# Kernel tuning notes

Hardware: AMD Instinct MI355X
Metric: run time of the kernel (lower is better)

The kernel has to match this reference:

```python
import math
import jax, jax.numpy as jnp
import numpy as np

B, S, HID, NH = 1, 2048, 4096, 32
HD = HID // NH  # 128
INV_NORM = 1.0 / math.sqrt(HD)


def _build_alibi(n_heads, seq_len, batch):
    # Standard Bloom ALiBi slopes.
    cp2 = 2 ** math.floor(math.log2(n_heads))
    base = 2.0 ** (-(2.0 ** -(math.log2(cp2) - 3)))
    slopes = base ** np.arange(1, cp2 + 1)
    if cp2 != n_heads:
        extra_base = 2.0 ** (-(2.0 ** -(math.log2(2 * cp2) - 3)))
        n_rem = min(cp2, n_heads - cp2)
        slopes = np.concatenate([slopes, extra_base ** np.arange(1, 2 * n_rem + 1, 2)])
    arange = np.arange(seq_len, dtype=np.float32)[None, None, :]
    alibi = slopes[:, None, None].astype(np.float32) * arange  # [NH,1,S]
    alibi = np.broadcast_to(alibi[None], (batch, n_heads, 1, seq_len)).reshape(batch * n_heads, 1, seq_len)
    return jnp.asarray(alibi, jnp.float32)


def setup_inputs() -> dict:
    key = jax.random.key(0)
    ks = jax.random.split(key, 5)
    return {
        "hidden_states": jax.random.normal(ks[0], (B, S, HID), jnp.float32),
        "alibi": _build_alibi(NH, S, B),  # [B*NH, 1, S]
        "w_qkv": jax.random.normal(ks[1], (3 * HID, HID), jnp.float32) * 0.02,
        "b_qkv": jax.random.normal(ks[2], (3 * HID,), jnp.float32) * 0.02,
        "w_dense": jax.random.normal(ks[3], (HID, HID), jnp.float32) * 0.02,
        "b_dense": jax.random.normal(ks[4], (HID,), jnp.float32) * 0.02,
    }


def reference(hidden_states, alibi, w_qkv, b_qkv, w_dense, b_dense):
    b, s, _ = hidden_states.shape
    # Fused QKV projection, per-head interleaved layout [B,S,NH,3,HD]
    fused = hidden_states @ w_qkv.T + b_qkv
    fused = fused.reshape(b, s, NH, 3, HD)
    q = fused[..., 0, :].transpose(0, 2, 1, 3).reshape(b * NH, s, HD)
    k = fused[..., 1, :].transpose(0, 2, 1, 3).reshape(b * NH, s, HD)
    v = fused[..., 2, :].transpose(0, 2, 1, 3).reshape(b * NH, s, HD)
    # baddbmm(alibi, q, k^T, beta=1.0, alpha=inv_norm_factor)
    scores = alibi + INV_NORM * jnp.einsum("bqd,bkd->bqk", q, k)  # [B*NH,S,S]
    causal = jnp.tril(jnp.ones((s, s), dtype=bool))
    scores = jnp.where(causal[None], scores, jnp.finfo(scores.dtype).min)
    probs = jax.nn.softmax(scores.astype(jnp.float32), axis=-1).astype(hidden_states.dtype)
    ctx = jnp.einsum("bqk,bkd->bqd", probs, v)  # [B*NH,S,HD]
    ctx = ctx.reshape(b, NH, s, HD).transpose(0, 2, 1, 3).reshape(b, s, HID)
    return ctx @ w_dense.T + b_dense
```

## Files before the change

### kernel.cpp

```cpp
#include <hip/hip_runtime.h>
#include <math.h>


typedef __attribute__((ext_vector_type(8))) short short8;
typedef __attribute__((ext_vector_type(4))) float floatx4;
typedef __attribute__((ext_vector_type(4))) unsigned short ushort4v;

#define S_LEN 2048
#define HID_DIM 4096
#define NHEADS 32
#define HDIM 128
#define QKV_N 12288
#define QK_STRIDE 8192
#define INV_NORM 0.08838834764831845f

__device__ __forceinline__ unsigned short f2bf(float f) {
    union { float f; unsigned int i; } v; v.f = f;
    unsigned int u = v.i;
    return (unsigned short)((u + 0x7fffu + ((u >> 16) & 1u)) >> 16);
}

typedef __attribute__((address_space(1))) unsigned int guint;
typedef __attribute__((address_space(3))) unsigned int luint;
__device__ __forceinline__ void gl_lds16(const unsigned short* g, unsigned short* l) {
    __builtin_amdgcn_global_load_lds((guint*)g, (luint*)l, 16, 0, 0);
}

__device__ __forceinline__ void wvm8() { asm volatile("s_waitcnt vmcnt(8)" ::: "memory"); }
__device__ __forceinline__ void wvm6() { asm volatile("s_waitcnt vmcnt(6)" ::: "memory"); }
__device__ __forceinline__ void wvm4() { asm volatile("s_waitcnt vmcnt(4)" ::: "memory"); }
__device__ __forceinline__ void wvm3() { asm volatile("s_waitcnt vmcnt(3)" ::: "memory"); }
__device__ __forceinline__ void wvm0() { asm volatile("s_waitcnt vmcnt(0)" ::: "memory"); }

__device__ __forceinline__ void phase_bar() {
    __builtin_amdgcn_s_barrier();
    __builtin_amdgcn_sched_barrier(0);
}

__global__ __launch_bounds__(256) void cvt_bf16(
    const float* __restrict__ src, unsigned short* __restrict__ dst)
{
    size_t i = ((size_t)blockIdx.x * 256 + threadIdx.x) * 8;
    float4 x = *(const float4*)(src + i);
    float4 y = *(const float4*)(src + i + 4);
    union { unsigned u[4]; short8 s; } r;
    r.u[0] = (unsigned)f2bf(x.x) | ((unsigned)f2bf(x.y) << 16);
    r.u[1] = (unsigned)f2bf(x.z) | ((unsigned)f2bf(x.w) << 16);
    r.u[2] = (unsigned)f2bf(y.x) | ((unsigned)f2bf(y.y) << 16);
    r.u[3] = (unsigned)f2bf(y.z) | ((unsigned)f2bf(y.w) << 16);
    *(short8*)(dst + i) = r.s;
}

template <int MODE, int BM>
__global__ __launch_bounds__(512, 2) void gemm_pipe(
    const unsigned short* __restrict__ A,
    const unsigned short* __restrict__ B,
    const float* __restrict__ bias,
    unsigned short* __restrict__ Cq,
    float* __restrict__ Cf,
    unsigned short* __restrict__ vt,
    int M, int N, int K)
{
    constexpr int BN = 256;
    constexpr int BK = 32;
    constexpr int MF = BM / 32;
    constexpr int WR = BM / 2;
    constexpr int BUFSH = (BM + BN) * BK;
    constexpr int LA = (BM * BK * 2) / 8192;

    __shared__ unsigned short lds[4 * BUFSH];

    const int t = threadIdx.x;
    const int w = t >> 6, lane = t & 63, quad = lane >> 4, l15 = lane & 15;
    const int wr = w >> 2, wc = w & 3;

    const int gx = gridDim.x;
    const int nwg = gx * gridDim.y;
    const int wg = blockIdx.y * gx + blockIdx.x;
    const int swz = (wg & 7) * (nwg >> 3) + (wg >> 3);
    const int bx = swz % gx, by = swz / gx;
    const int mb = by * BM, nb = bx * BN;

    const int srow = w * 16 + (lane >> 2);
    const int schunk = (((lane & 3) ^ ((lane >> 2) & 3)) << 3);
    const unsigned short* pa = A + (size_t)(mb + srow) * K + schunk;
    const unsigned short* pb = B + (size_t)(nb + srow) * K + schunk;
    const int la_off = w * 512;
    const int lb_off = BM * BK + w * 512;

    const int fchunk = ((quad ^ (l15 & 3)) << 3);
    const int aoff = (wr * WR + l15) * BK + fchunk;
    const int boff = BM * BK + (wc * 64 + l15) * BK + fchunk;

    floatx4 acc[MF][4];
#pragma unroll
    for (int i = 0; i < MF; i++)
#pragma unroll
        for (int j = 0; j < 4; j++) acc[i][j] = (floatx4)0.0f;

    int kstage = 0;
    auto stage = [&](int bufi) {
        unsigned short* lb = &lds[bufi * BUFSH];
#pragma unroll
        for (int i = 0; i < LA; i++)
            gl_lds16(pa + kstage + (size_t)i * 128 * K, lb + la_off + i * 4096);
        gl_lds16(pb + kstage, lb + lb_off);
        gl_lds16(pb + kstage + (size_t)128 * K, lb + lb_off + 4096);
        kstage += BK;
    };
    auto compute = [&](int bufi) {
        const unsigned short* lt = &lds[bufi * BUFSH];
        short8 af[MF], bfr[4];
#pragma unroll
        for (int m = 0; m < MF; m++)
            af[m] = *(const short8*)&lt[aoff + m * 16 * BK];
#pragma unroll
        for (int n = 0; n < 4; n++)
            bfr[n] = *(const short8*)&lt[boff + n * 16 * BK];
        __builtin_amdgcn_s_setprio(1);
#pragma unroll
        for (int m = 0; m < MF; m++)
#pragma unroll
            for (int n = 0; n < 4; n++)
                acc[m][n] = __builtin_amdgcn_mfma_f32_16x16x32_bf16(af[m], bfr[n], acc[m][n], 0, 0, 0);
        __builtin_amdgcn_s_setprio(0);
    };

    const int NT = K / BK;

    stage(0); stage(1); stage(2);

    for (int kt = 0; kt < NT - 2; kt++) {
        if constexpr (BM == 256) wvm8(); else wvm6();
        phase_bar();
        if (kt < NT - 3) stage((kt + 3) & 3);
        compute(kt & 3);
    }
    if constexpr (BM == 256) wvm4(); else wvm3();
    phase_bar();
    compute((NT - 2) & 3);
    wvm0();
    phase_bar();
    compute((NT - 1) & 3);

    if (MODE == 1) {
#pragma unroll
        for (int j = 0; j < 4; j++) {
            int cb = nb + wc * 64 + j * 16;
            int h = cb / 384;
            int type = (cb >> 7) % 3;
            int db = cb & 127;
            float bv = bias[cb + l15];
            if (type == 2) {
                unsigned short* vp = vt + ((size_t)h * HDIM + db + l15) * S_LEN;
#pragma unroll
                for (int m = 0; m < MF; m++) {
                    int rowbase = mb + wr * WR + m * 16 + quad * 4;
                    ushort4v pk;
#pragma unroll
                    for (int r = 0; r < 4; r++) pk[r] = f2bf(acc[m][j][r] + bv);
                    *(ushort4v*)&vp[rowbase] = pk;
                }
            } else {
                size_t colo = (size_t)h * 256 + type * 128 + db + l15;
#pragma unroll
                for (int m = 0; m < MF; m++) {
                    int rowbase = mb + wr * WR + m * 16 + quad * 4;
#pragma unroll
                    for (int r = 0; r < 4; r++)
                        Cq[(size_t)(rowbase + r) * QK_STRIDE + colo] =
                            f2bf(acc[m][j][r] + bv);
                }
            }
        }
    } else {
#pragma unroll
        for (int j = 0; j < 4; j++) {
            int col = nb + wc * 64 + j * 16 + l15;
            float bv = bias[col];
#pragma unroll
            for (int m = 0; m < MF; m++) {
                int rowbase = mb + wr * WR + m * 16 + quad * 4;
#pragma unroll
                for (int r = 0; r < 4; r++)
                    Cf[(size_t)(rowbase + r) * N + col] = acc[m][j][r] + bv;
            }
        }
    }
}

__global__ __launch_bounds__(256) void attn_flash(
    const unsigned short* __restrict__ qk,
    const unsigned short* __restrict__ vt,
    const float* __restrict__ alibi,
    unsigned short* __restrict__ ctx)
{
    __shared__ unsigned short k_lds[64 * 136];
    __shared__ unsigned short vt_lds[128 * 72];
    __shared__ unsigned short p_lds[4 * 16 * 72];

    int h = blockIdx.x;
    int qb = blockIdx.y * 64;
    int t = threadIdx.x;
    int w = t >> 6, lane = t & 63, quad = lane >> 4, l15 = lane & 15;
    int qoff = h * 256;

    short8 qf[4];
    {
        int qrow = qb + w * 16 + l15;
        const unsigned short* qp = qk + (size_t)qrow * QK_STRIDE + qoff;
        for (int ks = 0; ks < 4; ks++)
            qf[ks] = *(const short8*)&qp[ks * 32 + quad * 8];
    }

    floatx4 o[8];
    for (int j = 0; j < 8; j++) o[j] = (floatx4)0.0f;
    float m_prev[4], l_prev[4];
    for (int r = 0; r < 4; r++) { m_prev[r] = -INFINITY; l_prev[r] = 0.0f; }

    int ntiles = qb / 64 + 1;
    for (int tile = 0; tile < ntiles; tile++) {
        int kb = tile * 64;
        for (int i = 0; i < 4; i++) {
            int idx = t + 256 * i;
            int krow = idx >> 4, kcol = (idx & 15) * 8;
            *(short8*)&k_lds[krow * 136 + kcol] =
                *(const short8*)(qk + (size_t)(kb + krow) * QK_STRIDE + qoff + 128 + kcol);
            int d = idx >> 3, ch = (idx & 7) * 8;
            *(short8*)&vt_lds[d * 72 + ch] =
                *(const short8*)(vt + ((size_t)h * HDIM + d) * S_LEN + kb + ch);
        }
        __syncthreads();

        floatx4 s[4];
        for (int j = 0; j < 4; j++) s[j] = (floatx4)0.0f;
        for (int ks = 0; ks < 4; ks++) {
            for (int j = 0; j < 4; j++) {
                short8 bfr = *(const short8*)&k_lds[(j * 16 + l15) * 136 + ks * 32 + quad * 8];
                s[j] = __builtin_amdgcn_mfma_f32_16x16x32_bf16(qf[ks], bfr, s[j], 0, 0, 0);
            }
        }

        float sv[4][4];
        for (int j = 0; j < 4; j++) {
            int kcol = kb + j * 16 + l15;
            float al = alibi[h * S_LEN + kcol];
            for (int r = 0; r < 4; r++) {
                int qrow = qb + w * 16 + quad * 4 + r;
                float x = s[j][r] * INV_NORM + al;
                sv[j][r] = (kcol <= qrow) ? x : -INFINITY;
            }
        }

        float p[4][4];
        for (int r = 0; r < 4; r++) {
            float mt = fmaxf(fmaxf(sv[0][r], sv[1][r]), fmaxf(sv[2][r], sv[3][r]));
            for (int off = 1; off < 16; off <<= 1)
                mt = fmaxf(mt, __shfl_xor(mt, off, 64));
            float m_new = fmaxf(m_prev[r], mt);
            float alpha = __expf(m_prev[r] - m_new);
            float rs = 0.0f;
            for (int j = 0; j < 4; j++) {
                float pv = __expf(sv[j][r] - m_new);
                p[j][r] = pv;
                rs += pv;
            }
            for (int off = 1; off < 16; off <<= 1)
                rs += __shfl_xor(rs, off, 64);
            l_prev[r] = l_prev[r] * alpha + rs;
            m_prev[r] = m_new;
            for (int j = 0; j < 8; j++) o[j][r] *= alpha;
        }

        {
            unsigned short* pb = &p_lds[w * 16 * 72];
            for (int j = 0; j < 4; j++)
                for (int r = 0; r < 4; r++)
                    pb[(quad * 4 + r) * 72 + j * 16 + l15] = f2bf(p[j][r]);
        }
        {
            const unsigned short* pb = &p_lds[w * 16 * 72];
            for (int ks = 0; ks < 2; ks++) {
                short8 ap = *(const short8*)&pb[l15 * 72 + ks * 32 + quad * 8];
                for (int j = 0; j < 8; j++) {
                    short8 bv = *(const short8*)&vt_lds[(j * 16 + l15) * 72 + ks * 32 + quad * 8];
                    o[j] = __builtin_amdgcn_mfma_f32_16x16x32_bf16(ap, bv, o[j], 0, 0, 0);
                }
            }
        }
        __syncthreads();
    }

    for (int r = 0; r < 4; r++) {
        float linv = 1.0f / l_prev[r];
        int qrow = qb + w * 16 + quad * 4 + r;
        unsigned short* op = ctx + (size_t)qrow * HID_DIM + h * HDIM;
        for (int j = 0; j < 8; j++)
            op[j * 16 + l15] = f2bf(o[j][r] * linv);
    }
}

extern "C" void kernel_launch(void* const* d_in, const int* in_sizes, int n_in,
                              void* d_out, int out_size, void* d_ws, size_t ws_size,
                              hipStream_t stream) {
    const float* hidden  = (const float*)d_in[0];
    const float* alibi   = (const float*)d_in[1];
    const float* w_qkv   = (const float*)d_in[2];
    const float* b_qkv   = (const float*)d_in[3];
    const float* w_dense = (const float*)d_in[4];
    const float* b_dense = (const float*)d_in[5];
    float* out = (float*)d_out;

    unsigned short* ws    = (unsigned short*)d_ws;
    unsigned short* wq_bf = ws;
    unsigned short* fused = ws + (size_t)50331648;
    unsigned short* vt    = fused + (size_t)S_LEN * QK_STRIDE;
    unsigned short* hbf   = vt + (size_t)NHEADS * HDIM * S_LEN;
    unsigned short* ctx   = hbf;
    unsigned short* wd_bf = wq_bf;

    dim3 blk(256), blk512(512);
    cvt_bf16<<<dim3(4096),  blk, 0, stream>>>(hidden,  hbf);
    cvt_bf16<<<dim3(24576), blk, 0, stream>>>(w_qkv,   wq_bf);
    gemm_pipe<1, 256><<<dim3(QKV_N / 256, S_LEN / 256), blk512, 0, stream>>>(
        hbf, wq_bf, b_qkv, fused, nullptr, vt, S_LEN, QKV_N, HID_DIM);
    attn_flash<<<dim3(NHEADS, S_LEN / 64), blk, 0, stream>>>(fused, vt, alibi, ctx);
    cvt_bf16<<<dim3(8192), blk, 0, stream>>>(w_dense, wd_bf);
    gemm_pipe<0, 128><<<dim3(HID_DIM / 256, S_LEN / 128), blk512, 0, stream>>>(
        ctx, wd_bf, b_dense, nullptr, out, nullptr, S_LEN, HID_DIM, HID_DIM);
}
```

Before: 795.0 us.

## Retile QKV GEMM to BN=192, change LDS swizzle, prefetch K/V tiles in attention

The QKV GEMM tile width becomes a template parameter and is set to 192, giving 64x8=512 workgroups instead of 48x8, which may balance the 256-CU machine better. Only some waves issue the second B load, with per-wave waitcnt values to match. The LDS chunk swizzle changes to reduce bank conflicts. The attention kernel launches query tiles in reverse so the longest causal blocks start first, and it prefetches the next K/V tile into registers while the current one is computed, replacing the trailing __syncthreads with lgkm-wait barriers. This costs extra registers, and the per-wave waitcnt split depends on the hi-wave bookkeeping being correct.

```diff
diff --git a/kernel.cpp b/kernel.cpp
--- a/kernel.cpp
+++ b/kernel.cpp
@@ -33,6 +33,12 @@
 __device__ __forceinline__ void wvm0() { asm volatile("s_waitcnt vmcnt(0)" ::: "memory"); }
 
 __device__ __forceinline__ void phase_bar() {
+    __builtin_amdgcn_s_barrier();
+    __builtin_amdgcn_sched_barrier(0);
+}
+
+__device__ __forceinline__ void bar_lgkm() {
+    asm volatile("s_waitcnt lgkmcnt(0)" ::: "memory");
     __builtin_amdgcn_s_barrier();
     __builtin_amdgcn_sched_barrier(0);
 }
@@ -51,7 +57,7 @@
     *(short8*)(dst + i) = r.s;
 }
 
-template <int MODE, int BM>
+template <int MODE, int BM, int BN>
 __global__ __launch_bounds__(512, 2) void gemm_pipe(
     const unsigned short* __restrict__ A,
     const unsigned short* __restrict__ B,
@@ -61,18 +67,21 @@
     unsigned short* __restrict__ vt,
     int M, int N, int K)
 {
-    constexpr int BN = 256;
     constexpr int BK = 32;
     constexpr int MF = BM / 32;
+    constexpr int NF = BN / 64;
     constexpr int WR = BM / 2;
+    constexpr int WC = BN / 4;
     constexpr int BUFSH = (BM + BN) * BK;
-    constexpr int LA = (BM * BK * 2) / 8192;
+    constexpr int LA = BM / 128;
+    constexpr int BW2 = (BN - 128) / 16;
 
     __shared__ unsigned short lds[4 * BUFSH];
 
     const int t = threadIdx.x;
     const int w = t >> 6, lane = t & 63, quad = lane >> 4, l15 = lane & 15;
     const int wr = w >> 2, wc = w & 3;
+    const bool hi = (w < BW2);
 
     const int gx = gridDim.x;
     const int nwg = gx * gridDim.y;
@@ -82,21 +91,21 @@
     const int mb = by * BM, nb = bx * BN;
 
     const int srow = w * 16 + (lane >> 2);
-    const int schunk = (((lane & 3) ^ ((lane >> 2) & 3)) << 3);
+    const int schunk = (((lane & 3) ^ ((lane >> 3) & 3)) << 3);
     const unsigned short* pa = A + (size_t)(mb + srow) * K + schunk;
     const unsigned short* pb = B + (size_t)(nb + srow) * K + schunk;
     const int la_off = w * 512;
     const int lb_off = BM * BK + w * 512;
 
-    const int fchunk = ((quad ^ (l15 & 3)) << 3);
+    const int fchunk = ((quad ^ ((l15 >> 1) & 3)) << 3);
     const int aoff = (wr * WR + l15) * BK + fchunk;
-    const int boff = BM * BK + (wc * 64 + l15) * BK + fchunk;
-
-    floatx4 acc[MF][4];
+    const int boff = BM * BK + (wc * WC + l15) * BK + fchunk;
+
+    floatx4 acc[MF][NF];
 #pragma unroll
     for (int i = 0; i < MF; i++)
 #pragma unroll
-        for (int j = 0; j < 4; j++) acc[i][j] = (floatx4)0.0f;
+        for (int j = 0; j < NF; j++) acc[i][j] = (floatx4)0.0f;
 
     int kstage = 0;
     auto stage = [&](int bufi) {
@@ -105,38 +114,46 @@
         for (int i = 0; i < LA; i++)
             gl_lds16(pa + kstage + (size_t)i * 128 * K, lb + la_off + i * 4096);
         gl_lds16(pb + kstage, lb + lb_off);
-        gl_lds16(pb + kstage + (size_t)128 * K, lb + lb_off + 4096);
+        if (hi) gl_lds16(pb + kstage + (size_t)128 * K, lb + lb_off + 4096);
         kstage += BK;
     };
     auto compute = [&](int bufi) {
         const unsigned short* lt = &lds[bufi * BUFSH];
-        short8 af[MF], bfr[4];
+        short8 af[MF], bfr[NF];
 #pragma unroll
         for (int m = 0; m < MF; m++)
             af[m] = *(const short8*)&lt[aoff + m * 16 * BK];
 #pragma unroll
-        for (int n = 0; n < 4; n++)
+        for (int n = 0; n < NF; n++)
             bfr[n] = *(const short8*)&lt[boff + n * 16 * BK];
         __builtin_amdgcn_s_setprio(1);
 #pragma unroll
         for (int m = 0; m < MF; m++)
 #pragma unroll
-            for (int n = 0; n < 4; n++)
+            for (int n = 0; n < NF; n++)
                 acc[m][n] = __builtin_amdgcn_mfma_f32_16x16x32_bf16(af[m], bfr[n], acc[m][n], 0, 0, 0);
         __builtin_amdgcn_s_setprio(0);
     };
+    auto wait_steady = [&] {
+        if constexpr (LA == 2) { if (hi) wvm8(); else wvm6(); }
+        else wvm6();
+    };
+    auto wait_tail = [&] {
+        if constexpr (LA == 2) { if (hi) wvm4(); else wvm3(); }
+        else wvm3();
+    };
 
     const int NT = K / BK;
 
     stage(0); stage(1); stage(2);
 
     for (int kt = 0; kt < NT - 2; kt++) {
-        if constexpr (BM == 256) wvm8(); else wvm6();
+        wait_steady();
         phase_bar();
         if (kt < NT - 3) stage((kt + 3) & 3);
         compute(kt & 3);
     }
-    if constexpr (BM == 256) wvm4(); else wvm3();
+    wait_tail();
     phase_bar();
     compute((NT - 2) & 3);
     wvm0();
@@ -145,8 +162,8 @@
 
     if (MODE == 1) {
 #pragma unroll
-        for (int j = 0; j < 4; j++) {
-            int cb = nb + wc * 64 + j * 16;
+        for (int j = 0; j < NF; j++) {
+            int cb = nb + wc * WC + j * 16;
             int h = cb / 384;
             int type = (cb >> 7) % 3;
             int db = cb & 127;
@@ -175,8 +192,8 @@
         }
     } else {
 #pragma unroll
-        for (int j = 0; j < 4; j++) {
-            int col = nb + wc * 64 + j * 16 + l15;
+        for (int j = 0; j < NF; j++) {
+            int col = nb + wc * WC + j * 16 + l15;
             float bv = bias[col];
 #pragma unroll
             for (int m = 0; m < MF; m++) {
@@ -200,7 +217,8 @@
     __shared__ unsigned short p_lds[4 * 16 * 72];
 
     int h = blockIdx.x;
-    int qb = blockIdx.y * 64;
+    int qt = (int)gridDim.y - 1 - (int)blockIdx.y;
+    int qb = qt * 64;
     int t = threadIdx.x;
     int w = t >> 6, lane = t & 63, quad = lane >> 4, l15 = lane & 15;
     int qoff = h * 256;
@@ -218,19 +236,34 @@
     float m_prev[4], l_prev[4];
     for (int r = 0; r < 4; r++) { m_prev[r] = -INFINITY; l_prev[r] = 0.0f; }
 
-    int ntiles = qb / 64 + 1;
+    int krow[4], kcol[4], vd[4], vch[4];
+    for (int i = 0; i < 4; i++) {
+        int idx = t + 256 * i;
+        krow[i] = idx >> 4; kcol[i] = (idx & 15) * 8;
+        vd[i]   = idx >> 3; vch[i] = (idx & 7) * 8;
+    }
+    short8 kreg[4], vreg[4];
+    auto prefetch = [&](int tile) {
+        int kb = tile * 64;
+#pragma unroll
+        for (int i = 0; i < 4; i++) {
+            kreg[i] = *(const short8*)(qk + (size_t)(kb + krow[i]) * QK_STRIDE + qoff + 128 + kcol[i]);
+            vreg[i] = *(const short8*)(vt + ((size_t)h * HDIM + vd[i]) * S_LEN + kb + vch[i]);
+        }
+    };
+
+    int ntiles = qt + 1;
+    prefetch(0);
     for (int tile = 0; tile < ntiles; tile++) {
+        bar_lgkm();
+#pragma unroll
+        for (int i = 0; i < 4; i++) {
+            *(short8*)&k_lds[krow[i] * 136 + kcol[i]] = kreg[i];
+            *(short8*)&vt_lds[vd[i] * 72 + vch[i]]    = vreg[i];
+        }
+        if (tile + 1 < ntiles) prefetch(tile + 1);
+        bar_lgkm();
         int kb = tile * 64;
-        for (int i = 0; i < 4; i++) {
-            int idx = t + 256 * i;
-            int krow = idx >> 4, kcol = (idx & 15) * 8;
-            *(short8*)&k_lds[krow * 136 + kcol] =
-                *(const short8*)(qk + (size_t)(kb + krow) * QK_STRIDE + qoff + 128 + kcol);
-            int d = idx >> 3, ch = (idx & 7) * 8;
-            *(short8*)&vt_lds[d * 72 + ch] =
-                *(const short8*)(vt + ((size_t)h * HDIM + d) * S_LEN + kb + ch);
-        }
-        __syncthreads();
 
         floatx4 s[4];
         for (int j = 0; j < 4; j++) s[j] = (floatx4)0.0f;
@@ -243,12 +276,12 @@
 
         float sv[4][4];
         for (int j = 0; j < 4; j++) {
-            int kcol = kb + j * 16 + l15;
-            float al = alibi[h * S_LEN + kcol];
+            int kcol2 = kb + j * 16 + l15;
+            float al = alibi[h * S_LEN + kcol2];
             for (int r = 0; r < 4; r++) {
                 int qrow = qb + w * 16 + quad * 4 + r;
                 float x = s[j][r] * INV_NORM + al;
-                sv[j][r] = (kcol <= qrow) ? x : -INFINITY;
+                sv[j][r] = (kcol2 <= qrow) ? x : -INFINITY;
             }
         }
 
@@ -288,7 +321,6 @@
                 }
             }
         }
-        __syncthreads();
     }
 
     for (int r = 0; r < 4; r++) {
@@ -322,10 +354,10 @@
     dim3 blk(256), blk512(512);
     cvt_bf16<<<dim3(4096),  blk, 0, stream>>>(hidden,  hbf);
     cvt_bf16<<<dim3(24576), blk, 0, stream>>>(w_qkv,   wq_bf);
-    gemm_pipe<1, 256><<<dim3(QKV_N / 256, S_LEN / 256), blk512, 0, stream>>>(
+    gemm_pipe<1, 256, 192><<<dim3(QKV_N / 192, S_LEN / 256), blk512, 0, stream>>>(
         hbf, wq_bf, b_qkv, fused, nullptr, vt, S_LEN, QKV_N, HID_DIM);
     attn_flash<<<dim3(NHEADS, S_LEN / 64), blk, 0, stream>>>(fused, vt, alibi, ctx);
     cvt_bf16<<<dim3(8192), blk, 0, stream>>>(w_dense, wd_bf);
-    gemm_pipe<0, 128><<<dim3(HID_DIM / 256, S_LEN / 128), blk512, 0, stream>>>(
+    gemm_pipe<0, 128, 256><<<dim3(HID_DIM / 256, S_LEN / 128), blk512, 0, stream>>>(
         ctx, wd_bf, b_dense, nullptr, out, nullptr, S_LEN, HID_DIM, HID_DIM);
 }
```

After: 721.5 us. 9.2% less time.
